# Performance work log

Hardware: AMD Instinct MI355X
Metric: run time of the kernel (lower is better)

## Reference

```python
import jax, jax.numpy as jnp
import numpy as np

N_NODES = 50000
N_EDGES = 1000000
D_NODE = 64
D_EDGE = 64


def setup_inputs() -> dict:
    key = jax.random.key(0)
    ks = jax.random.split(key, 12)
    d, de = D_NODE, D_EDGE
    din = 2 * d + de
    s = lambda f_in: 1.0 / np.sqrt(f_in)
    return {
        "node_feat": jax.random.normal(ks[0], (N_NODES, d), jnp.float32),
        "edge_src": jax.random.randint(ks[1], (N_EDGES,), 0, N_NODES, jnp.int32),
        "edge_dst": jax.random.randint(ks[2], (N_EDGES,), 0, N_NODES, jnp.int32),
        "edge_feat": jax.random.normal(ks[3], (N_EDGES, de), jnp.float32),
        # msg_mlp: Linear(din,d) -> SiLU -> Linear(d,d)
        "W_m1": jax.random.uniform(ks[4], (din, d), jnp.float32, -s(din), s(din)),
        "b_m1": jax.random.uniform(ks[5], (d,), jnp.float32, -s(din), s(din)),
        "W_m2": jax.random.uniform(ks[6], (d, d), jnp.float32, -s(d), s(d)),
        "b_m2": jax.random.uniform(ks[7], (d,), jnp.float32, -s(d), s(d)),
        # update_mlp: Linear(d,d) -> SiLU -> Linear(d,d)
        "W_u1": jax.random.uniform(ks[8], (d, d), jnp.float32, -s(d), s(d)),
        "b_u1": jax.random.uniform(ks[9], (d,), jnp.float32, -s(d), s(d)),
        "W_u2": jax.random.uniform(ks[10], (d, d), jnp.float32, -s(d), s(d)),
        "b_u2": jax.random.uniform(ks[11], (d,), jnp.float32, -s(d), s(d)),
        # LayerNorm params
        "ln_gamma": jnp.ones((d,), jnp.float32),
        "ln_beta": jnp.zeros((d,), jnp.float32),
    }


def _layer_norm(x, gamma, beta, eps=1e-5):
    mu = jnp.mean(x, axis=-1, keepdims=True)
    var = jnp.var(x, axis=-1, keepdims=True)
    return (x - mu) * jax.lax.rsqrt(var + eps) * gamma + beta


def reference(node_feat, edge_src, edge_dst, edge_feat,
              W_m1, b_m1, W_m2, b_m2, W_u1, b_u1, W_u2, b_u2,
              ln_gamma, ln_beta):
    # gather endpoint features per edge: [E, 2d+de]
    msg_input = jnp.concatenate(
        [node_feat[edge_src], node_feat[edge_dst], edge_feat], axis=-1)
    h = jax.nn.silu(msg_input @ W_m1 + b_m1)
    messages = h @ W_m2 + b_m2                      # [E, d]
    aggregated = jax.ops.segment_sum(messages, edge_dst,
                                     num_segments=node_feat.shape[0])
    upd = jax.nn.silu(aggregated @ W_u1 + b_u1) @ W_u2 + b_u2
    return _layer_norm(node_feat + upd, ln_gamma, ln_beta)
```

## Files before the change

### kernel.cpp

```cpp
#include <hip/hip_runtime.h>
#include <stdint.h>

typedef __bf16 bf16;
typedef __attribute__((ext_vector_type(8))) bf16 bf16x8;
typedef __attribute__((ext_vector_type(4))) float f32x4;

#define D 64
#define EPW 32

__device__ __forceinline__ float silu_f(float x) {
    return x / (1.0f + __expf(-x));
}

__global__ void cvt_nf_kernel(const float* __restrict__ nf, bf16* __restrict__ nfb,
                              int* __restrict__ cnt, int total8, int N) {
    const int i = blockIdx.x * blockDim.x + threadIdx.x;
    if (i < total8) {
        f32x4 a = ((const f32x4*)nf)[i*2], b = ((const f32x4*)nf)[i*2 + 1];
        bf16x8 v;
        #pragma unroll
        for (int k = 0; k < 4; ++k) { v[k] = (bf16)a[k]; v[4+k] = (bf16)b[k]; }
        ((bf16x8*)nfb)[i] = v;
    }
    for (int j = blockIdx.x * blockDim.x + threadIdx.x; j < N; j += gridDim.x * blockDim.x)
        cnt[j] = 0;
}

__global__ void hist_kernel(const int* __restrict__ edst, int* __restrict__ cnt, int E) {
    const int stride = gridDim.x * blockDim.x;
    for (int e = blockIdx.x * blockDim.x + threadIdx.x; e < E; e += stride)
        atomicAdd(&cnt[edst[e]], 1);
}

__global__ void scan_part_kernel(const int* __restrict__ cnt, int* __restrict__ part, int N) {
    __shared__ int red[256];
    const int t = threadIdx.x, idx = blockIdx.x * 256 + t;
    red[t] = (idx < N) ? cnt[idx] : 0;
    __syncthreads();
    for (int off = 128; off; off >>= 1) {
        if (t < off) red[t] += red[t + off];
        __syncthreads();
    }
    if (t == 0) part[blockIdx.x] = red[0];
}

__global__ void scan_base_kernel(int* __restrict__ part, int nblk) {
    __shared__ int sc[256];
    const int t = threadIdx.x;
    const int v = (t < nblk) ? part[t] : 0;
    sc[t] = v;
    __syncthreads();
    for (int off = 1; off < 256; off <<= 1) {
        int u = (t >= off) ? sc[t - off] : 0;
        __syncthreads();
        sc[t] += u;
        __syncthreads();
    }
    part[t] = sc[t] - v;
}

__global__ void scan_fin_kernel(const int* __restrict__ cnt, const int* __restrict__ part,
                                int* __restrict__ cur, float* __restrict__ outz, int N) {
    __shared__ int sc[256];
    const int t = threadIdx.x, idx = blockIdx.x * 256 + t;
    const int v = (idx < N) ? cnt[idx] : 0;
    sc[t] = v;
    __syncthreads();
    for (int off = 1; off < 256; off <<= 1) {
        int u = (t >= off) ? sc[t - off] : 0;
        __syncthreads();
        sc[t] += u;
        __syncthreads();
    }
    if (idx < N) {
        cur[idx] = sc[t] - v + part[blockIdx.x];
        f32x4 z = {0.f, 0.f, 0.f, 0.f};
        float* o = outz + (size_t)idx * D;
        #pragma unroll
        for (int i = 0; i < 16; ++i) ((f32x4*)o)[i] = z;
    }
}

__global__ void scatter_kernel(const int* __restrict__ esrc, const int* __restrict__ edst,
                               int* __restrict__ cur, int4* __restrict__ sde, int E) {
    const int stride = gridDim.x * blockDim.x;
    for (int e = blockIdx.x * blockDim.x + threadIdx.x; e < E; e += stride) {
        const int d = edst[e];
        const int pos = atomicAdd(&cur[d], 1);
        sde[pos] = make_int4(esrc[e], d, e, 0);
    }
}

__launch_bounds__(512, 4)
__global__ void mp_edge_sorted_kernel(
    const bf16* __restrict__ nfb,
    const int4* __restrict__ sde,
    const float* __restrict__ efeat,
    const float* __restrict__ W1, const float* __restrict__ b1,
    const float* __restrict__ W2, const float* __restrict__ b2,
    float* __restrict__ agg,
    int E)
{
    __shared__ __align__(16) bf16 W1f[6*4*64*8];
    __shared__ __align__(16) bf16 W2f[2*4*64*8];
    __shared__ __align__(16) bf16 HM[8][32*72];
    __shared__ float b1s[D], b2s[D];

    const int t    = threadIdx.x;
    const int lane = t & 63;
    const int w    = t >> 6;
    const int g    = lane >> 4;
    const int c    = lane & 15;

    for (int idx = t; idx < 6*4*64; idx += 512) {
        int l = idx & 63, nt = (idx >> 6) & 3, ks = idx >> 8;
        int k0 = ks*32 + (l >> 4)*8, col = nt*16 + (l & 15);
        bf16x8 v;
        #pragma unroll
        for (int i = 0; i < 8; ++i) v[i] = (bf16)W1[(k0 + i)*D + col];
        *(bf16x8*)&W1f[idx*8] = v;
    }
    for (int idx = t; idx < 2*4*64; idx += 512) {
        int l = idx & 63, nt = (idx >> 6) & 3, ks = idx >> 8;
        int k0 = ks*32 + (l >> 4)*8, col = nt*16 + (l & 15);
        bf16x8 v;
        #pragma unroll
        for (int i = 0; i < 8; ++i) v[i] = (bf16)W2[(k0 + i)*D + col];
        *(bf16x8*)&W2f[idx*8] = v;
    }
    if (t < D) { b1s[t] = b1[t]; b2s[t] = b2[t]; }
    __syncthreads();

    bf16* hm = &HM[w][0];
    const int nwt = (E + EPW - 1) / EPW;
    const int t0 = blockIdx.x*8 + w;
    const int tstride = gridDim.x*8;

    int4 nq0 = make_int4(0,0,0,0), nq1 = make_int4(0,0,0,0);
    if (t0 < nwt) {
        nq0 = sde[min(t0*EPW + c,      E - 1)];
        nq1 = sde[min(t0*EPW + 16 + c, E - 1)];
    }

    for (int tile = t0; tile < nwt; tile += tstride) {
        const int e0 = tile * EPW;
        const int4 q0 = nq0, q1 = nq1;
        const int tn = tile + tstride;
        if (tn < nwt) {
            nq0 = sde[min(tn*EPW + c,      E - 1)];
            nq1 = sde[min(tn*EPW + 16 + c, E - 1)];
        }
        const int se0 = q0.x, de0 = q0.y, ee0 = q0.z;
        const int se1 = q1.x, de1 = q1.y, ee1 = q1.z;

        bf16x8 an[8];
        f32x4  ef[8];
        #pragma unroll
        for (int ks = 0; ks < 4; ++ks) {
            const int row0 = (ks < 2) ? se0 : de0;
            const int row1 = (ks < 2) ? se1 : de1;
            const int coff = (ks & 1)*32 + g*8;
            an[ks*2]   = *(const bf16x8*)&nfb[(size_t)row0*D + coff];
            an[ks*2+1] = *(const bf16x8*)&nfb[(size_t)row1*D + coff];
        }
        #pragma unroll
        for (int ks2 = 0; ks2 < 2; ++ks2) {
            const int coff = ks2*32 + g*8;
            const float* p0 = efeat + (size_t)ee0*D + coff;
            const float* p1 = efeat + (size_t)ee1*D + coff;
            ef[ks2*4+0] = ((const f32x4*)p0)[0];
            ef[ks2*4+1] = ((const f32x4*)p0)[1];
            ef[ks2*4+2] = ((const f32x4*)p1)[0];
            ef[ks2*4+3] = ((const f32x4*)p1)[1];
        }

        f32x4 acc0[4] = {f32x4{0,0,0,0}, f32x4{0,0,0,0}, f32x4{0,0,0,0}, f32x4{0,0,0,0}};
        f32x4 acc1[4] = {f32x4{0,0,0,0}, f32x4{0,0,0,0}, f32x4{0,0,0,0}, f32x4{0,0,0,0}};
        #pragma unroll
        for (int ks = 0; ks < 4; ++ks) {
            #pragma unroll
            for (int n = 0; n < 4; ++n) {
                bf16x8 bb = *(const bf16x8*)&W1f[((ks*4 + n)*64 + lane)*8];
                acc0[n] = __builtin_amdgcn_mfma_f32_16x16x32_bf16(an[ks*2],   bb, acc0[n], 0, 0, 0);
                acc1[n] = __builtin_amdgcn_mfma_f32_16x16x32_bf16(an[ks*2+1], bb, acc1[n], 0, 0, 0);
            }
        }
        #pragma unroll
        for (int ks2 = 0; ks2 < 2; ++ks2) {
            bf16x8 a0, a1;
            #pragma unroll
            for (int i = 0; i < 4; ++i) {
                a0[i]   = (bf16)ef[ks2*4+0][i];
                a0[4+i] = (bf16)ef[ks2*4+1][i];
                a1[i]   = (bf16)ef[ks2*4+2][i];
                a1[4+i] = (bf16)ef[ks2*4+3][i];
            }
            #pragma unroll
            for (int n = 0; n < 4; ++n) {
                bf16x8 bb = *(const bf16x8*)&W1f[(((ks2+4)*4 + n)*64 + lane)*8];
                acc0[n] = __builtin_amdgcn_mfma_f32_16x16x32_bf16(a0, bb, acc0[n], 0, 0, 0);
                acc1[n] = __builtin_amdgcn_mfma_f32_16x16x32_bf16(a1, bb, acc1[n], 0, 0, 0);
            }
        }

        #pragma unroll
        for (int n = 0; n < 4; ++n) {
            const int col = n*16 + c;
            const float bias = b1s[col];
            #pragma unroll
            for (int j = 0; j < 4; ++j) {
                hm[(g*4 + j)*72 + col]      = (bf16)silu_f(acc0[n][j] + bias);
                hm[(16 + g*4 + j)*72 + col] = (bf16)silu_f(acc1[n][j] + bias);
            }
        }

        f32x4 acc2a[4] = {f32x4{0,0,0,0}, f32x4{0,0,0,0}, f32x4{0,0,0,0}, f32x4{0,0,0,0}};
        f32x4 acc2b[4] = {f32x4{0,0,0,0}, f32x4{0,0,0,0}, f32x4{0,0,0,0}, f32x4{0,0,0,0}};
        #pragma unroll
        for (int ks = 0; ks < 2; ++ks) {
            bf16x8 a0 = *(const bf16x8*)&hm[c*72        + ks*32 + g*8];
            bf16x8 a1 = *(const bf16x8*)&hm[(16 + c)*72 + ks*32 + g*8];
            #pragma unroll
            for (int n = 0; n < 4; ++n) {
                bf16x8 bb = *(const bf16x8*)&W2f[((ks*4 + n)*64 + lane)*8];
                acc2a[n] = __builtin_amdgcn_mfma_f32_16x16x32_bf16(a0, bb, acc2a[n], 0, 0, 0);
                acc2b[n] = __builtin_amdgcn_mfma_f32_16x16x32_bf16(a1, bb, acc2b[n], 0, 0, 0);
            }
        }

        asm volatile("s_waitcnt lgkmcnt(0)" ::: "memory");

        #pragma unroll
        for (int n = 0; n < 4; ++n) {
            const int col = n*16 + c;
            const float bias = b2s[col];
            #pragma unroll
            for (int j = 0; j < 4; ++j) {
                hm[(g*4 + j)*72 + col]      = (bf16)(acc2a[n][j] + bias);
                hm[(16 + g*4 + j)*72 + col] = (bf16)(acc2b[n][j] + bias);
            }
        }

        const int da = __shfl(de0, lane & 15);
        const int db = __shfl(de1, lane & 15);
        const int row = lane & 31;
        int rowd = (lane & 16) ? db : da;
        if (e0 + row >= E) rowd = -1;
        const int prevd = __shfl(rowd, (lane + 63) & 63);
        const bool st = (row == 0) || (rowd != prevd);
        unsigned long long m = __ballot(st) & 0xFFFFFFFFull;

        while (m) {
            const int a = __builtin_ctzll(m); m &= m - 1;
            const int rb = m ? __builtin_ctzll(m) : 32;
            const int d = __shfl(rowd, a);
            if (d >= 0) {
                float s = 0.f;
                for (int r = a; r < rb; ++r) s += (float)hm[r*72 + lane];
                float* dp = &agg[(size_t)d*D + lane];
                if (a > 0 && rb < 32) *dp = s;
                else atomicAdd(dp, s);
            }
        }
    }
}

__launch_bounds__(256, 3)
__global__ void mp_edge_atomic_kernel(
    const float* __restrict__ node_feat,
    const int*   __restrict__ esrc,
    const int*   __restrict__ edst,
    const float* __restrict__ efeat,
    const float* __restrict__ W1, const float* __restrict__ b1,
    const float* __restrict__ W2, const float* __restrict__ b2,
    float* __restrict__ agg,
    int E)
{
    __shared__ __align__(16) bf16 W1f[6*4*64*8];
    __shared__ __align__(16) bf16 W2f[2*4*64*8];
    __shared__ __align__(16) bf16 HM[4][32*72];
    __shared__ float b1s[D], b2s[D];

    const int t    = threadIdx.x;
    const int lane = t & 63;
    const int w    = t >> 6;
    const int g    = lane >> 4;
    const int c    = lane & 15;

    for (int idx = t; idx < 6*4*64; idx += 256) {
        int l = idx & 63, nt = (idx >> 6) & 3, ks = idx >> 8;
        int k0 = ks*32 + (l >> 4)*8, col = nt*16 + (l & 15);
        bf16x8 v;
        #pragma unroll
        for (int i = 0; i < 8; ++i) v[i] = (bf16)W1[(k0 + i)*D + col];
        *(bf16x8*)&W1f[idx*8] = v;
    }
    for (int idx = t; idx < 2*4*64; idx += 256) {
        int l = idx & 63, nt = (idx >> 6) & 3, ks = idx >> 8;
        int k0 = ks*32 + (l >> 4)*8, col = nt*16 + (l & 15);
        bf16x8 v;
        #pragma unroll
        for (int i = 0; i < 8; ++i) v[i] = (bf16)W2[(k0 + i)*D + col];
        *(bf16x8*)&W2f[idx*8] = v;
    }
    if (t < D) { b1s[t] = b1[t]; b2s[t] = b2[t]; }
    __syncthreads();

    bf16* hm = &HM[w][0];
    const int nwt = (E + EPW - 1) / EPW;

    for (int tile = blockIdx.x*4 + w; tile < nwt; tile += gridDim.x*4) {
        const int e0 = tile * EPW;
        const int r0 = min(e0 + c,      E - 1);
        const int r1 = min(e0 + 16 + c, E - 1);
        const int se0 = esrc[r0], de0 = edst[r0];
        const int se1 = esrc[r1], de1 = edst[r1];

        f32x4 acc0[4] = {f32x4{0,0,0,0}, f32x4{0,0,0,0}, f32x4{0,0,0,0}, f32x4{0,0,0,0}};
        f32x4 acc1[4] = {f32x4{0,0,0,0}, f32x4{0,0,0,0}, f32x4{0,0,0,0}, f32x4{0,0,0,0}};
        #pragma unroll
        for (int ks = 0; ks < 6; ++ks) {
            const int col = ks*32 + g*8;
            const float *p0, *p1;
            if (col < 64)       { p0 = node_feat + (size_t)se0*D + col;        p1 = node_feat + (size_t)se1*D + col; }
            else if (col < 128) { p0 = node_feat + (size_t)de0*D + (col - 64); p1 = node_feat + (size_t)de1*D + (col - 64); }
            else                { p0 = efeat + (size_t)r0*D + (col - 128);     p1 = efeat + (size_t)r1*D + (col - 128); }
            f32x4 xa = ((const f32x4*)p0)[0], xb = ((const f32x4*)p0)[1];
            f32x4 ya = ((const f32x4*)p1)[0], yb = ((const f32x4*)p1)[1];
            bf16x8 a0, a1;
            #pragma unroll
            for (int i = 0; i < 4; ++i) {
                a0[i] = (bf16)xa[i];  a0[4+i] = (bf16)xb[i];
                a1[i] = (bf16)ya[i];  a1[4+i] = (bf16)yb[i];
            }
            #pragma unroll
            for (int n = 0; n < 4; ++n) {
                bf16x8 bb = *(const bf16x8*)&W1f[((ks*4 + n)*64 + lane)*8];
                acc0[n] = __builtin_amdgcn_mfma_f32_16x16x32_bf16(a0, bb, acc0[n], 0, 0, 0);
                acc1[n] = __builtin_amdgcn_mfma_f32_16x16x32_bf16(a1, bb, acc1[n], 0, 0, 0);
            }
        }

        #pragma unroll
        for (int n = 0; n < 4; ++n) {
            const int col = n*16 + c;
            const float bias = b1s[col];
            #pragma unroll
            for (int j = 0; j < 4; ++j) {
                hm[(g*4 + j)*72 + col]      = (bf16)silu_f(acc0[n][j] + bias);
                hm[(16 + g*4 + j)*72 + col] = (bf16)silu_f(acc1[n][j] + bias);
            }
        }

        f32x4 acc2a[4] = {f32x4{0,0,0,0}, f32x4{0,0,0,0}, f32x4{0,0,0,0}, f32x4{0,0,0,0}};
        f32x4 acc2b[4] = {f32x4{0,0,0,0}, f32x4{0,0,0,0}, f32x4{0,0,0,0}, f32x4{0,0,0,0}};
        #pragma unroll
        for (int ks = 0; ks < 2; ++ks) {
            bf16x8 a0 = *(const bf16x8*)&hm[c*72        + ks*32 + g*8];
            bf16x8 a1 = *(const bf16x8*)&hm[(16 + c)*72 + ks*32 + g*8];
            #pragma unroll
            for (int n = 0; n < 4; ++n) {
                bf16x8 bb = *(const bf16x8*)&W2f[((ks*4 + n)*64 + lane)*8];
                acc2a[n] = __builtin_amdgcn_mfma_f32_16x16x32_bf16(a0, bb, acc2a[n], 0, 0, 0);
                acc2b[n] = __builtin_amdgcn_mfma_f32_16x16x32_bf16(a1, bb, acc2b[n], 0, 0, 0);
            }
        }

        #pragma unroll
        for (int j = 0; j < 4; ++j) {
            const int row = g*4 + j;
            const int d0 = __shfl(de0, row);
            const int d1 = __shfl(de1, row);
            const bool ok0 = (e0 + row)      < E;
            const bool ok1 = (e0 + 16 + row) < E;
            #pragma unroll
            for (int n = 0; n < 4; ++n) {
                const int col = n*16 + c;
                if (ok0) atomicAdd(&agg[(size_t)d0*D + col], acc2a[n][j] + b2s[col]);
                if (ok1) atomicAdd(&agg[(size_t)d1*D + col], acc2b[n][j] + b2s[col]);
            }
        }
    }
}

__launch_bounds__(256, 4)
__global__ void node_gemm_kernel(
    const float* __restrict__ node_feat,
    const float* __restrict__ Wu1, const float* __restrict__ bu1,
    const float* __restrict__ Wu2, const float* __restrict__ bu2,
    const float* __restrict__ gamma, const float* __restrict__ beta,
    float* __restrict__ inout, int N)
{
    __shared__ __align__(16) bf16 Wf1[2*4*64*8];
    __shared__ __align__(16) bf16 Wf2[2*4*64*8];
    __shared__ __align__(16) bf16 Hs[4][16*72];
    __shared__ float b1s[D], b2s[D], gs[D], bs[D];

    const int t    = threadIdx.x;
    const int lane = t & 63;
    const int w    = t >> 6;
    const int g    = lane >> 4;
    const int c    = lane & 15;

    for (int idx = t; idx < 2*4*64; idx += 256) {
        int l = idx & 63, nt = (idx >> 6) & 3, ks = idx >> 8;
        int k0 = ks*32 + (l >> 4)*8, col = nt*16 + (l & 15);
        bf16x8 v1, v2;
        #pragma unroll
        for (int i = 0; i < 8; ++i) {
            v1[i] = (bf16)Wu1[(k0 + i)*D + col];
            v2[i] = (bf16)Wu2[(k0 + i)*D + col];
        }
        *(bf16x8*)&Wf1[idx*8] = v1;
        *(bf16x8*)&Wf2[idx*8] = v2;
    }
    if (t < D) { b1s[t] = bu1[t]; b2s[t] = bu2[t]; gs[t] = gamma[t]; bs[t] = beta[t]; }
    __syncthreads();

    const int base = blockIdx.x*64 + w*16;
    if (base >= N) return;
    bf16* hs = &Hs[w][0];

    f32x4 acc[4] = {f32x4{0,0,0,0}, f32x4{0,0,0,0}, f32x4{0,0,0,0}, f32x4{0,0,0,0}};
    #pragma unroll
    for (int ks = 0; ks < 2; ++ks) {
        const int rowA = min(base + c, N - 1);
        const float* p = inout + (size_t)rowA*D + ks*32 + g*8;
        f32x4 xa = ((const f32x4*)p)[0], xb = ((const f32x4*)p)[1];
        bf16x8 a;
        #pragma unroll
        for (int i = 0; i < 4; ++i) { a[i] = (bf16)xa[i]; a[4+i] = (bf16)xb[i]; }
        #pragma unroll
        for (int n = 0; n < 4; ++n) {
            bf16x8 bb = *(const bf16x8*)&Wf1[((ks*4 + n)*64 + lane)*8];
            acc[n] = __builtin_amdgcn_mfma_f32_16x16x32_bf16(a, bb, acc[n], 0, 0, 0);
        }
    }
    #pragma unroll
    for (int n = 0; n < 4; ++n) {
        const int col = n*16 + c;
        const float bias = b1s[col];
        #pragma unroll
        for (int j = 0; j < 4; ++j)
            hs[(g*4 + j)*72 + col] = (bf16)silu_f(acc[n][j] + bias);
    }

    f32x4 acc2[4] = {f32x4{0,0,0,0}, f32x4{0,0,0,0}, f32x4{0,0,0,0}, f32x4{0,0,0,0}};
    #pragma unroll
    for (int ks = 0; ks < 2; ++ks) {
        bf16x8 a = *(const bf16x8*)&hs[c*72 + ks*32 + g*8];
        #pragma unroll
        for (int n = 0; n < 4; ++n) {
            bf16x8 bb = *(const bf16x8*)&Wf2[((ks*4 + n)*64 + lane)*8];
            acc2[n] = __builtin_amdgcn_mfma_f32_16x16x32_bf16(a, bb, acc2[n], 0, 0, 0);
        }
    }

    float y[4][4];
    #pragma unroll
    for (int n = 0; n < 4; ++n) {
        const int col = n*16 + c;
        #pragma unroll
        for (int j = 0; j < 4; ++j) {
            const int row = base + g*4 + j;
            const float x0 = (row < N) ? node_feat[(size_t)row*D + col] : 0.f;
            y[n][j] = x0 + acc2[n][j] + b2s[col];
        }
    }
    #pragma unroll
    for (int j = 0; j < 4; ++j) {
        float s1 = 0.f, s2 = 0.f;
        #pragma unroll
        for (int n = 0; n < 4; ++n) { s1 += y[n][j]; s2 += y[n][j]*y[n][j]; }
        #pragma unroll
        for (int mm = 1; mm < 16; mm <<= 1) {
            s1 += __shfl_xor(s1, mm);
            s2 += __shfl_xor(s2, mm);
        }
        const float mu  = s1 * (1.0f/64.0f);
        const float var = s2 * (1.0f/64.0f) - mu*mu;
        const float rs  = rsqrtf(var + 1e-5f);
        const int row = base + g*4 + j;
        if (row < N) {
            #pragma unroll
            for (int n = 0; n < 4; ++n) {
                const int col = n*16 + c;
                inout[(size_t)row*D + col] = (y[n][j] - mu)*rs*gs[col] + bs[col];
            }
        }
    }
}

extern "C" void kernel_launch(void* const* d_in, const int* in_sizes, int n_in,
                              void* d_out, int out_size, void* d_ws, size_t ws_size,
                              hipStream_t stream) {
    const float* node_feat = (const float*)d_in[0];
    const int*   esrc      = (const int*)d_in[1];
    const int*   edst      = (const int*)d_in[2];
    const float* efeat     = (const float*)d_in[3];
    const float* W_m1      = (const float*)d_in[4];
    const float* b_m1      = (const float*)d_in[5];
    const float* W_m2      = (const float*)d_in[6];
    const float* b_m2      = (const float*)d_in[7];
    const float* W_u1      = (const float*)d_in[8];
    const float* b_u1      = (const float*)d_in[9];
    const float* W_u2      = (const float*)d_in[10];
    const float* b_u2      = (const float*)d_in[11];
    const float* ln_gamma  = (const float*)d_in[12];
    const float* ln_beta   = (const float*)d_in[13];

    float* out = (float*)d_out;
    const int E = in_sizes[1];
    const int N = in_sizes[0] / D;

    const size_t sde_bytes = (((size_t)E * 16) + 255) & ~(size_t)255;
    const size_t int_bytes = ((sizeof(int) * (2*(size_t)N + 256)) + 255) & ~(size_t)255;
    const size_t nfb_bytes = (((size_t)N * D * 2) + 255) & ~(size_t)255;
    const size_t need = sde_bytes + int_bytes + nfb_bytes;

    const int nwt    = (E + EPW - 1) / EPW;
    const int gridN  = (N + 63) / 64;
    const int nchunk = (N + 255) / 256;

    if (ws_size >= need) {
        int4* sde  = (int4*)d_ws;
        int*  cnt  = (int*)((char*)d_ws + sde_bytes);
        int*  cur  = cnt + N;
        int*  part = cur + N;
        bf16* nfb  = (bf16*)((char*)d_ws + sde_bytes + int_bytes);

        const int total8 = N * D / 8;
        cvt_nf_kernel   <<<(total8 + 255)/256, 256, 0, stream>>>(node_feat, nfb, cnt, total8, N);
        hist_kernel     <<<1024, 256, 0, stream>>>(edst, cnt, E);
        scan_part_kernel<<<nchunk, 256, 0, stream>>>(cnt, part, N);
        scan_base_kernel<<<1, 256, 0, stream>>>(part, nchunk);
        scan_fin_kernel <<<nchunk, 256, 0, stream>>>(cnt, part, cur, out, N);
        scatter_kernel  <<<1024, 256, 0, stream>>>(esrc, edst, cur, sde, E);

        const int nblk8 = (nwt + 7) / 8;
        const int grid1 = nblk8 < 512 ? nblk8 : 512;
        mp_edge_sorted_kernel<<<grid1, 512, 0, stream>>>(nfb, sde, efeat,
                                                         W_m1, b_m1, W_m2, b_m2,
                                                         out, E);
    } else {
        hipMemsetAsync(out, 0, (size_t)N * D * sizeof(float), stream);
        const int nblk4 = (nwt + 3) / 4;
        const int grid1 = nblk4 < 768 ? nblk4 : 768;
        mp_edge_atomic_kernel<<<grid1, 256, 0, stream>>>(node_feat, esrc, edst, efeat,
                                                         W_m1, b_m1, W_m2, b_m2,
                                                         out, E);
    }

    node_gemm_kernel<<<gridN, 256, 0, stream>>>(node_feat, W_u1, b_u1, W_u2, b_u2,
                                                ln_gamma, ln_beta, out, N);
}
```

Baseline: 238.3 us.

## Give waves contiguous tile chunks and prefetch next tile's source rows

The sorted edge kernel now hands each wave a contiguous run of tiles instead of striding across the grid. The loop is unrolled by two with double-buffered registers, so the next tile's edge records and source-node gathers are issued before the current tile's MFMA work. The count clear moves to a memset, and the bf16 conversion and histogram kernels are fused into one launch. This is meant to hide gather latency and cut a launch, at the cost of more registers and a possible imbalance on the last chunk of tiles.

```diff
diff --git a/kernel.cpp b/kernel.cpp
--- a/kernel.cpp
+++ b/kernel.cpp
@@ -12,8 +12,9 @@
     return x / (1.0f + __expf(-x));
 }
 
-__global__ void cvt_nf_kernel(const float* __restrict__ nf, bf16* __restrict__ nfb,
-                              int* __restrict__ cnt, int total8, int N) {
+__global__ void cvt_hist_kernel(const float* __restrict__ nf, bf16* __restrict__ nfb,
+                                const int* __restrict__ edst, int* __restrict__ cnt,
+                                int total8, int E) {
     const int i = blockIdx.x * blockDim.x + threadIdx.x;
     if (i < total8) {
         f32x4 a = ((const f32x4*)nf)[i*2], b = ((const f32x4*)nf)[i*2 + 1];
@@ -22,13 +23,8 @@
         for (int k = 0; k < 4; ++k) { v[k] = (bf16)a[k]; v[4+k] = (bf16)b[k]; }
         ((bf16x8*)nfb)[i] = v;
     }
-    for (int j = blockIdx.x * blockDim.x + threadIdx.x; j < N; j += gridDim.x * blockDim.x)
-        cnt[j] = 0;
-}
-
-__global__ void hist_kernel(const int* __restrict__ edst, int* __restrict__ cnt, int E) {
     const int stride = gridDim.x * blockDim.x;
-    for (int e = blockIdx.x * blockDim.x + threadIdx.x; e < E; e += stride)
+    for (int e = i; e < E; e += stride)
         atomicAdd(&cnt[edst[e]], 1);
 }
 
@@ -99,7 +95,7 @@
     const float* __restrict__ W1, const float* __restrict__ b1,
     const float* __restrict__ W2, const float* __restrict__ b2,
     float* __restrict__ agg,
-    int E)
+    int E, int cpw)
 {
     __shared__ __align__(16) bf16 W1f[6*4*64*8];
     __shared__ __align__(16) bf16 W2f[2*4*64*8];
@@ -132,137 +128,152 @@
     __syncthreads();
 
     bf16* hm = &HM[w][0];
-    const int nwt = (E + EPW - 1) / EPW;
-    const int t0 = blockIdx.x*8 + w;
-    const int tstride = gridDim.x*8;
-
-    int4 nq0 = make_int4(0,0,0,0), nq1 = make_int4(0,0,0,0);
-    if (t0 < nwt) {
-        nq0 = sde[min(t0*EPW + c,      E - 1)];
-        nq1 = sde[min(t0*EPW + 16 + c, E - 1)];
-    }
-
-    for (int tile = t0; tile < nwt; tile += tstride) {
-        const int e0 = tile * EPW;
-        const int4 q0 = nq0, q1 = nq1;
-        const int tn = tile + tstride;
-        if (tn < nwt) {
-            nq0 = sde[min(tn*EPW + c,      E - 1)];
-            nq1 = sde[min(tn*EPW + 16 + c, E - 1)];
-        }
-        const int se0 = q0.x, de0 = q0.y, ee0 = q0.z;
-        const int se1 = q1.x, de1 = q1.y, ee1 = q1.z;
-
-        bf16x8 an[8];
-        f32x4  ef[8];
-        #pragma unroll
-        for (int ks = 0; ks < 4; ++ks) {
-            const int row0 = (ks < 2) ? se0 : de0;
-            const int row1 = (ks < 2) ? se1 : de1;
-            const int coff = (ks & 1)*32 + g*8;
-            an[ks*2]   = *(const bf16x8*)&nfb[(size_t)row0*D + coff];
-            an[ks*2+1] = *(const bf16x8*)&nfb[(size_t)row1*D + coff];
-        }
-        #pragma unroll
-        for (int ks2 = 0; ks2 < 2; ++ks2) {
-            const int coff = ks2*32 + g*8;
-            const float* p0 = efeat + (size_t)ee0*D + coff;
-            const float* p1 = efeat + (size_t)ee1*D + coff;
-            ef[ks2*4+0] = ((const f32x4*)p0)[0];
-            ef[ks2*4+1] = ((const f32x4*)p0)[1];
-            ef[ks2*4+2] = ((const f32x4*)p1)[0];
-            ef[ks2*4+3] = ((const f32x4*)p1)[1];
-        }
-
-        f32x4 acc0[4] = {f32x4{0,0,0,0}, f32x4{0,0,0,0}, f32x4{0,0,0,0}, f32x4{0,0,0,0}};
-        f32x4 acc1[4] = {f32x4{0,0,0,0}, f32x4{0,0,0,0}, f32x4{0,0,0,0}, f32x4{0,0,0,0}};
-        #pragma unroll
-        for (int ks = 0; ks < 4; ++ks) {
-            #pragma unroll
-            for (int n = 0; n < 4; ++n) {
-                bf16x8 bb = *(const bf16x8*)&W1f[((ks*4 + n)*64 + lane)*8];
-                acc0[n] = __builtin_amdgcn_mfma_f32_16x16x32_bf16(an[ks*2],   bb, acc0[n], 0, 0, 0);
-                acc1[n] = __builtin_amdgcn_mfma_f32_16x16x32_bf16(an[ks*2+1], bb, acc1[n], 0, 0, 0);
-            }
-        }
-        #pragma unroll
-        for (int ks2 = 0; ks2 < 2; ++ks2) {
-            bf16x8 a0, a1;
-            #pragma unroll
-            for (int i = 0; i < 4; ++i) {
-                a0[i]   = (bf16)ef[ks2*4+0][i];
-                a0[4+i] = (bf16)ef[ks2*4+1][i];
-                a1[i]   = (bf16)ef[ks2*4+2][i];
-                a1[4+i] = (bf16)ef[ks2*4+3][i];
-            }
-            #pragma unroll
-            for (int n = 0; n < 4; ++n) {
-                bf16x8 bb = *(const bf16x8*)&W1f[(((ks2+4)*4 + n)*64 + lane)*8];
-                acc0[n] = __builtin_amdgcn_mfma_f32_16x16x32_bf16(a0, bb, acc0[n], 0, 0, 0);
-                acc1[n] = __builtin_amdgcn_mfma_f32_16x16x32_bf16(a1, bb, acc1[n], 0, 0, 0);
-            }
-        }
-
-        #pragma unroll
-        for (int n = 0; n < 4; ++n) {
-            const int col = n*16 + c;
-            const float bias = b1s[col];
-            #pragma unroll
-            for (int j = 0; j < 4; ++j) {
-                hm[(g*4 + j)*72 + col]      = (bf16)silu_f(acc0[n][j] + bias);
-                hm[(16 + g*4 + j)*72 + col] = (bf16)silu_f(acc1[n][j] + bias);
-            }
-        }
-
-        f32x4 acc2a[4] = {f32x4{0,0,0,0}, f32x4{0,0,0,0}, f32x4{0,0,0,0}, f32x4{0,0,0,0}};
-        f32x4 acc2b[4] = {f32x4{0,0,0,0}, f32x4{0,0,0,0}, f32x4{0,0,0,0}, f32x4{0,0,0,0}};
-        #pragma unroll
-        for (int ks = 0; ks < 2; ++ks) {
-            bf16x8 a0 = *(const bf16x8*)&hm[c*72        + ks*32 + g*8];
-            bf16x8 a1 = *(const bf16x8*)&hm[(16 + c)*72 + ks*32 + g*8];
-            #pragma unroll
-            for (int n = 0; n < 4; ++n) {
-                bf16x8 bb = *(const bf16x8*)&W2f[((ks*4 + n)*64 + lane)*8];
-                acc2a[n] = __builtin_amdgcn_mfma_f32_16x16x32_bf16(a0, bb, acc2a[n], 0, 0, 0);
-                acc2b[n] = __builtin_amdgcn_mfma_f32_16x16x32_bf16(a1, bb, acc2b[n], 0, 0, 0);
-            }
-        }
-
-        asm volatile("s_waitcnt lgkmcnt(0)" ::: "memory");
-
-        #pragma unroll
-        for (int n = 0; n < 4; ++n) {
-            const int col = n*16 + c;
-            const float bias = b2s[col];
-            #pragma unroll
-            for (int j = 0; j < 4; ++j) {
-                hm[(g*4 + j)*72 + col]      = (bf16)(acc2a[n][j] + bias);
-                hm[(16 + g*4 + j)*72 + col] = (bf16)(acc2b[n][j] + bias);
-            }
-        }
-
-        const int da = __shfl(de0, lane & 15);
-        const int db = __shfl(de1, lane & 15);
-        const int row = lane & 31;
-        int rowd = (lane & 16) ? db : da;
-        if (e0 + row >= E) rowd = -1;
-        const int prevd = __shfl(rowd, (lane + 63) & 63);
-        const bool st = (row == 0) || (rowd != prevd);
-        unsigned long long m = __ballot(st) & 0xFFFFFFFFull;
-
-        while (m) {
-            const int a = __builtin_ctzll(m); m &= m - 1;
-            const int rb = m ? __builtin_ctzll(m) : 32;
-            const int d = __shfl(rowd, a);
-            if (d >= 0) {
-                float s = 0.f;
-                for (int r = a; r < rb; ++r) s += (float)hm[r*72 + lane];
-                float* dp = &agg[(size_t)d*D + lane];
-                if (a > 0 && rb < 32) *dp = s;
-                else atomicAdd(dp, s);
-            }
-        }
-    }
+    const int nwt  = (E + EPW - 1) / EPW;
+    const int tbeg = (blockIdx.x*8 + w) * cpw;
+    const int tend = min(tbeg + cpw, nwt);
+    if (tbeg >= tend) return;
+
+    int4 q0 = sde[min(tbeg*EPW + c,      E - 1)];
+    int4 q1 = sde[min(tbeg*EPW + 16 + c, E - 1)];
+    bf16x8 sA0a = *(const bf16x8*)&nfb[(size_t)q0.x*D +      g*8];
+    bf16x8 sA0b = *(const bf16x8*)&nfb[(size_t)q0.x*D + 32 + g*8];
+    bf16x8 sA1a = *(const bf16x8*)&nfb[(size_t)q1.x*D +      g*8];
+    bf16x8 sA1b = *(const bf16x8*)&nfb[(size_t)q1.x*D + 32 + g*8];
+    bf16x8 sB0a, sB0b, sB1a, sB1b;
+
+#define TILE_BODY(T, CS0a, CS0b, CS1a, CS1b, NS0a, NS0b, NS1a, NS1b)           \
+{                                                                              \
+    const int e0 = (T) * EPW;                                                  \
+    const int tnx = ((T) + 1 < tend) ? (T) + 1 : (T);                          \
+                   \
+    const int ee0 = q0.z, ee1 = q1.z;                                          \
+    f32x4 ef[8];                                                               \
+    {                                                                          \
+        const float* p0 = efeat + (size_t)ee0*D + g*8;                         \
+        const float* p1 = efeat + (size_t)ee1*D + g*8;                         \
+        ef[0] = ((const f32x4*)p0)[0];  ef[1] = ((const f32x4*)p0)[1];         \
+        ef[2] = ((const f32x4*)p1)[0];  ef[3] = ((const f32x4*)p1)[1];         \
+        ef[4] = ((const f32x4*)(p0 + 32))[0]; ef[5] = ((const f32x4*)(p0 + 32))[1]; \
+        ef[6] = ((const f32x4*)(p1 + 32))[0]; ef[7] = ((const f32x4*)(p1 + 32))[1]; \
+    }                                                                          \
+           \
+    const int4 nq0 = sde[min(tnx*EPW + c,      E - 1)];                        \
+    const int4 nq1 = sde[min(tnx*EPW + 16 + c, E - 1)];                        \
+    NS0a = *(const bf16x8*)&nfb[(size_t)nq0.x*D +      g*8];                   \
+    NS0b = *(const bf16x8*)&nfb[(size_t)nq0.x*D + 32 + g*8];                   \
+    NS1a = *(const bf16x8*)&nfb[(size_t)nq1.x*D +      g*8];                   \
+    NS1b = *(const bf16x8*)&nfb[(size_t)nq1.x*D + 32 + g*8];                   \
+                         \
+    const bf16x8 ad0a = *(const bf16x8*)&nfb[(size_t)q0.y*D +      g*8];       \
+    const bf16x8 ad0b = *(const bf16x8*)&nfb[(size_t)q0.y*D + 32 + g*8];       \
+    const bf16x8 ad1a = *(const bf16x8*)&nfb[(size_t)q1.y*D +      g*8];       \
+    const bf16x8 ad1b = *(const bf16x8*)&nfb[(size_t)q1.y*D + 32 + g*8];       \
+                                                 \
+    f32x4 acc0[4] = {f32x4{0,0,0,0}, f32x4{0,0,0,0}, f32x4{0,0,0,0}, f32x4{0,0,0,0}}; \
+    f32x4 acc1[4] = {f32x4{0,0,0,0}, f32x4{0,0,0,0}, f32x4{0,0,0,0}, f32x4{0,0,0,0}}; \
+    _Pragma("unroll")                                                          \
+    for (int n = 0; n < 4; ++n) {                                              \
+        bf16x8 bb0 = *(const bf16x8*)&W1f[((0*4 + n)*64 + lane)*8];            \
+        bf16x8 bb1 = *(const bf16x8*)&W1f[((1*4 + n)*64 + lane)*8];            \
+        acc0[n] = __builtin_amdgcn_mfma_f32_16x16x32_bf16(CS0a, bb0, acc0[n], 0, 0, 0); \
+        acc1[n] = __builtin_amdgcn_mfma_f32_16x16x32_bf16(CS1a, bb0, acc1[n], 0, 0, 0); \
+        acc0[n] = __builtin_amdgcn_mfma_f32_16x16x32_bf16(CS0b, bb1, acc0[n], 0, 0, 0); \
+        acc1[n] = __builtin_amdgcn_mfma_f32_16x16x32_bf16(CS1b, bb1, acc1[n], 0, 0, 0); \
+    }                                                                          \
+    _Pragma("unroll")                                                          \
+    for (int n = 0; n < 4; ++n) {                                              \
+        bf16x8 bb2 = *(const bf16x8*)&W1f[((2*4 + n)*64 + lane)*8];            \
+        bf16x8 bb3 = *(const bf16x8*)&W1f[((3*4 + n)*64 + lane)*8];            \
+        acc0[n] = __builtin_amdgcn_mfma_f32_16x16x32_bf16(ad0a, bb2, acc0[n], 0, 0, 0); \
+        acc1[n] = __builtin_amdgcn_mfma_f32_16x16x32_bf16(ad1a, bb2, acc1[n], 0, 0, 0); \
+        acc0[n] = __builtin_amdgcn_mfma_f32_16x16x32_bf16(ad0b, bb3, acc0[n], 0, 0, 0); \
+        acc1[n] = __builtin_amdgcn_mfma_f32_16x16x32_bf16(ad1b, bb3, acc1[n], 0, 0, 0); \
+    }                                                                          \
+    _Pragma("unroll")                                                          \
+    for (int ks2 = 0; ks2 < 2; ++ks2) {                                        \
+        bf16x8 a0, a1;                                                         \
+        _Pragma("unroll")                                                      \
+        for (int i = 0; i < 4; ++i) {                                          \
+            a0[i]   = (bf16)ef[ks2*4+0][i];                                    \
+            a0[4+i] = (bf16)ef[ks2*4+1][i];                                    \
+            a1[i]   = (bf16)ef[ks2*4+2][i];                                    \
+            a1[4+i] = (bf16)ef[ks2*4+3][i];                                    \
+        }                                                                      \
+        _Pragma("unroll")                                                      \
+        for (int n = 0; n < 4; ++n) {                                          \
+            bf16x8 bb = *(const bf16x8*)&W1f[(((ks2+4)*4 + n)*64 + lane)*8];   \
+            acc0[n] = __builtin_amdgcn_mfma_f32_16x16x32_bf16(a0, bb, acc0[n], 0, 0, 0); \
+            acc1[n] = __builtin_amdgcn_mfma_f32_16x16x32_bf16(a1, bb, acc1[n], 0, 0, 0); \
+        }                                                                      \
+    }                                                                          \
+                                               \
+    _Pragma("unroll")                                                          \
+    for (int n = 0; n < 4; ++n) {                                              \
+        const int col = n*16 + c;                                              \
+        const float bias = b1s[col];                                           \
+        _Pragma("unroll")                                                      \
+        for (int j = 0; j < 4; ++j) {                                          \
+            hm[(g*4 + j)*72 + col]      = (bf16)silu_f(acc0[n][j] + bias);     \
+            hm[(16 + g*4 + j)*72 + col] = (bf16)silu_f(acc1[n][j] + bias);     \
+        }                                                                      \
+    }                                                                          \
+                                                   \
+    f32x4 acc2a[4] = {f32x4{0,0,0,0}, f32x4{0,0,0,0}, f32x4{0,0,0,0}, f32x4{0,0,0,0}}; \
+    f32x4 acc2b[4] = {f32x4{0,0,0,0}, f32x4{0,0,0,0}, f32x4{0,0,0,0}, f32x4{0,0,0,0}}; \
+    _Pragma("unroll")                                                          \
+    for (int ks = 0; ks < 2; ++ks) {                                           \
+        bf16x8 a0 = *(const bf16x8*)&hm[c*72        + ks*32 + g*8];            \
+        bf16x8 a1 = *(const bf16x8*)&hm[(16 + c)*72 + ks*32 + g*8];            \
+        _Pragma("unroll")                                                      \
+        for (int n = 0; n < 4; ++n) {                                          \
+            bf16x8 bb = *(const bf16x8*)&W2f[((ks*4 + n)*64 + lane)*8];        \
+            acc2a[n] = __builtin_amdgcn_mfma_f32_16x16x32_bf16(a0, bb, acc2a[n], 0, 0, 0); \
+            acc2b[n] = __builtin_amdgcn_mfma_f32_16x16x32_bf16(a1, bb, acc2b[n], 0, 0, 0); \
+        }                                                                      \
+    }                                                                          \
+    asm volatile("s_waitcnt lgkmcnt(0)" ::: "memory");                         \
+                                           \
+    _Pragma("unroll")                                                          \
+    for (int n = 0; n < 4; ++n) {                                              \
+        const int col = n*16 + c;                                              \
+        const float bias = b2s[col];                                           \
+        _Pragma("unroll")                                                      \
+        for (int j = 0; j < 4; ++j) {                                          \
+            hm[(g*4 + j)*72 + col]      = (bf16)(acc2a[n][j] + bias);          \
+            hm[(16 + g*4 + j)*72 + col] = (bf16)(acc2b[n][j] + bias);          \
+        }                                                                      \
+    }                                                                          \
+                                    \
+    const int da = __shfl(q0.y, lane & 15);                                    \
+    const int db = __shfl(q1.y, lane & 15);                                    \
+    const int row = lane & 31;                                                 \
+    int rowd = (lane & 16) ? db : da;                                          \
+    if (e0 + row >= E) rowd = -1;                                              \
+    const int prevd = __shfl(rowd, (lane + 63) & 63);                          \
+    const bool st = (row == 0) || (rowd != prevd);                             \
+    unsigned long long m = __ballot(st) & 0xFFFFFFFFull;                       \
+    while (m) {                                                                \
+        const int a = __builtin_ctzll(m); m &= m - 1;                          \
+        const int rb = m ? __builtin_ctzll(m) : 32;                            \
+        const int d = __shfl(rowd, a);                                         \
+        if (d >= 0) {                                                          \
+            float s = 0.f;                                                     \
+            for (int r = a; r < rb; ++r) s += (float)hm[r*72 + lane];          \
+            float* dp = &agg[(size_t)d*D + lane];                              \
+            if (a > 0 && rb < 32) *dp = s;                                     \
+            else atomicAdd(dp, s);                                             \
+        }                                                                      \
+    }                                                                          \
+    q0 = nq0; q1 = nq1;                                                        \
+}
+
+    for (int tt = tbeg; tt < tend; tt += 2) {
+        TILE_BODY(tt, sA0a, sA0b, sA1a, sA1b, sB0a, sB0b, sB1a, sB1b);
+        if (tt + 1 < tend) {
+            TILE_BODY(tt + 1, sB0a, sB0b, sB1a, sB1b, sA0a, sA0b, sA1a, sA1b);
+        }
+    }
+#undef TILE_BODY
 }
 
 __launch_bounds__(256, 3)
@@ -530,18 +541,19 @@
         bf16* nfb  = (bf16*)((char*)d_ws + sde_bytes + int_bytes);
 
         const int total8 = N * D / 8;
-        cvt_nf_kernel   <<<(total8 + 255)/256, 256, 0, stream>>>(node_feat, nfb, cnt, total8, N);
-        hist_kernel     <<<1024, 256, 0, stream>>>(edst, cnt, E);
+        hipMemsetAsync(cnt, 0, sizeof(int)*(size_t)N, stream);
+        cvt_hist_kernel <<<(total8 + 255)/256, 256, 0, stream>>>(node_feat, nfb, edst, cnt, total8, E);
         scan_part_kernel<<<nchunk, 256, 0, stream>>>(cnt, part, N);
         scan_base_kernel<<<1, 256, 0, stream>>>(part, nchunk);
         scan_fin_kernel <<<nchunk, 256, 0, stream>>>(cnt, part, cur, out, N);
         scatter_kernel  <<<1024, 256, 0, stream>>>(esrc, edst, cur, sde, E);
 
-        const int nblk8 = (nwt + 7) / 8;
-        const int grid1 = nblk8 < 512 ? nblk8 : 512;
+        const int grid1 = 512;
+        const int nwaves = grid1 * 8;
+        const int cpw = (nwt + nwaves - 1) / nwaves;
         mp_edge_sorted_kernel<<<grid1, 512, 0, stream>>>(nfb, sde, efeat,
                                                          W_m1, b_m1, W_m2, b_m2,
-                                                         out, E);
+                                                         out, E, cpw);
     } else {
         hipMemsetAsync(out, 0, (size_t)N * D * sizeof(float), stream);
         const int nblk4 = (nwt + 3) / 4;
```

Result: slower. 261.5 us (+9.7%).
